# Performance work log

Hardware: AMD Instinct MI355X
Metric: run time of the kernel (lower is better)

## Reference

```python
import jax, jax.numpy as jnp
import numpy as np

HEADS = 8
DHEAD = 64
A_SCALE = 8.0  # cosine-attention logit scale (a=8 in source)
ROPE_BASE = 10000.0


def _mp_weight(w, centered):
    # Magnitude-preserving (EDM2-style) weight: optional zero-mean over fan-in,
    # unit-norm per output row, scaled by 1/sqrt(fan_in).
    if centered:
        w = w - w.mean(axis=1, keepdims=True)
    w = w / (jnp.linalg.norm(w, axis=1, keepdims=True) + 1e-8)
    return w / jnp.sqrt(jnp.asarray(w.shape[1], w.dtype))


def _rope_cos_sin(Hs, Ws, d, dtype=jnp.float32):
    # 2D axial RoPE: first d/4 rotation pairs encode row position, last d/4 column position.
    quarter = d // 4
    freqs = 1.0 / (ROPE_BASE ** (jnp.arange(quarter, dtype=dtype) / quarter))  # [d/4]
    ah = jnp.arange(Hs, dtype=dtype)[:, None] * freqs                          # [H, d/4]
    aw = jnp.arange(Ws, dtype=dtype)[:, None] * freqs                          # [W, d/4]
    ang = jnp.concatenate([
        jnp.broadcast_to(ah[:, None, :], (Hs, Ws, quarter)),
        jnp.broadcast_to(aw[None, :, :], (Hs, Ws, quarter)),
    ], axis=-1).reshape(Hs * Ws, d // 2)                                       # [L, d/2]
    return jnp.cos(ang), jnp.sin(ang)


def _apply_rope(t, cos, sin):
    # t: [N, h, L, d]; rotate interleaved pairs.
    x1, x2 = t[..., 0::2], t[..., 1::2]
    r1 = x1 * cos - x2 * sin
    r2 = x1 * sin + x2 * cos
    return jnp.stack([r1, r2], axis=-1).reshape(t.shape)


def setup_inputs() -> dict:
    key = jax.random.key(0)
    ks = jax.random.split(key, 8)
    N, C, Hs, Ws = 8, 256, 32, 32
    E, Hc = 512, 512
    return {
        "x": jax.random.normal(ks[0], (N, C, Hs, Ws), jnp.float32),
        "w": jax.random.normal(ks[1], (N, E), jnp.float32),
        "InputGain": jax.random.uniform(ks[2], (3 * Hc,), jnp.float32),
        "ResidualGain": jax.random.uniform(ks[3], (C,), jnp.float32),
        "qkv_w": jax.random.normal(ks[4], (3 * Hc, C), jnp.float32),
        "qkv_b": jnp.zeros((3 * Hc,), jnp.float32),
        "mod_w": jax.random.normal(ks[5], (E, C), jnp.float32) / jnp.sqrt(512.0),
        "proj_w": jax.random.normal(ks[6], (C, Hc), jnp.float32),
        "sinks": jnp.zeros((HEADS,), jnp.float32),
    }


def reference(x, w, InputGain, ResidualGain, qkv_w, qkv_b, mod_w, proj_w, sinks):
    N, C, Hs, Ws = x.shape
    L = Hs * Ws
    Hc = qkv_w.shape[0] // 3

    # --- fused QKV: style-modulated, biased, centered 1x1 conv with per-out-channel gain ---
    style = w @ mod_w + 1.0                                   # [N, C]
    Wq = _mp_weight(qkv_w, centered=True)                     # [3Hc, C]
    xm = x * style[:, :, None, None]
    y = jnp.einsum('nchw,oc->nohw', xm, Wq)
    y = (y + qkv_b[None, :, None, None]) * InputGain[None, :, None, None]  # [N, 3Hc, H, W]

    # --- split heads, flatten space: [N, h, L, d] ---
    y = y.reshape(N, 3, HEADS, DHEAD, L)
    q = jnp.transpose(y[:, 0], (0, 1, 3, 2))
    k = jnp.transpose(y[:, 1], (0, 1, 3, 2))
    v = jnp.transpose(y[:, 2], (0, 1, 3, 2))

    # --- 2D RoPE on q, k ---
    cos, sin = _rope_cos_sin(Hs, Ws, DHEAD, x.dtype)
    q = _apply_rope(q, cos, sin)
    k = _apply_rope(k, cos, sin)

    # --- cosine attention with per-head sink logit ---
    qn = q / (jnp.linalg.norm(q, axis=-1, keepdims=True) + 1e-8)
    kn = k / (jnp.linalg.norm(k, axis=-1, keepdims=True) + 1e-8)
    logits = A_SCALE * jnp.einsum('nhld,nhmd->nhlm', qn, kn)  # [N, h, L, L]
    sink = jnp.broadcast_to(sinks[None, :, None, None], (N, HEADS, L, 1))
    probs = jax.nn.softmax(jnp.concatenate([logits, sink], axis=-1), axis=-1)[..., :L]
    o = jnp.einsum('nhlm,nhmd->nhld', probs, v)               # [N, h, L, d]

    # --- merge heads back to map, centered 1x1 projection with per-out-channel gain ---
    o = jnp.transpose(o, (0, 1, 3, 2)).reshape(N, Hc, Hs, Ws)
    Wp = _mp_weight(proj_w, centered=True) * ResidualGain[:, None]  # [C, Hc]
    out = jnp.einsum('nchw,oc->nohw', o, Wp)
    return x + out
```

## Files before the change

### kernel.cpp

```cpp
#include <hip/hip_runtime.h>
#include <hip/hip_bf16.h>
#include <math.h>

#define NN 8
#define CC 256
#define LL 1024
#define EE 512
#define HEADS 8
#define DH 64

#define OFF_STYLE   0u
#define OFF_BIAS    2048u
#define OFF_COS     3584u
#define OFF_SIN     36352u
#define OFF_WQB     69120u
#define OFF_WPB     265728u
#define OFF_XMT     331264u
#define OFF_Q       1379840u
#define OFF_K       3476992u
#define OFF_V       5574144u
#define OFF_O       7671296u

typedef __bf16 bf16x8 __attribute__((ext_vector_type(8)));
typedef __bf16 bf16x4 __attribute__((ext_vector_type(4)));
typedef short s16x4 __attribute__((ext_vector_type(4)));
typedef float f32x4 __attribute__((ext_vector_type(4)));

__global__ __launch_bounds__(256) void k_style(const float* __restrict__ w,
                                               const float* __restrict__ mod_w,
                                               float* __restrict__ style) {
    int n  = blockIdx.x >> 2;
    int cg = blockIdx.x & 3;
    int wv = threadIdx.x >> 6, lane = threadIdx.x & 63;
    int c = cg * 64 + lane;
    __shared__ float red[4][64];
    float acc = 0.f;
    #pragma unroll 8
    for (int e = wv * 128; e < wv * 128 + 128; ++e)
        acc += w[n * EE + e] * mod_w[e * CC + c];
    red[wv][lane] = acc;
    __syncthreads();
    if (wv == 0)
        style[n * CC + c] = red[0][lane] + red[1][lane] + red[2][lane] + red[3][lane] + 1.0f;
}

__global__ __launch_bounds__(256) void k_prep_wq(const float* __restrict__ qkv_w,
                                                 const float* __restrict__ gain,
                                                 const float* __restrict__ bias,
                                                 __hip_bfloat16* __restrict__ wqb,
                                                 float* __restrict__ biasg) {
    int wv = threadIdx.x >> 6, lane = threadIdx.x & 63;
    int o = blockIdx.x * 4 + wv;
    float4 v = *reinterpret_cast<const float4*>(qkv_w + o * CC + lane * 4);
    float s = v.x + v.y + v.z + v.w;
    #pragma unroll
    for (int off = 1; off < 64; off <<= 1) s += __shfl_xor(s, off);
    float mean = s * (1.0f / 256.0f);
    float c0 = v.x - mean, c1 = v.y - mean, c2 = v.z - mean, c3 = v.w - mean;
    float ss = c0 * c0 + c1 * c1 + c2 * c2 + c3 * c3;
    #pragma unroll
    for (int off = 1; off < 64; off <<= 1) ss += __shfl_xor(ss, off);
    float g = gain[o];
    float scale = g / ((sqrtf(ss) + 1e-8f) * 16.0f);
    bf16x4 outv;
    outv[0] = (__bf16)(c0 * scale); outv[1] = (__bf16)(c1 * scale);
    outv[2] = (__bf16)(c2 * scale); outv[3] = (__bf16)(c3 * scale);
    *reinterpret_cast<bf16x4*>((__bf16*)wqb + o * CC + lane * 4) = outv;
    if (lane == 0) biasg[o] = bias[o] * g;
}

__global__ __launch_bounds__(256) void k_prep_wp(const float* __restrict__ proj_w,
                                                 const float* __restrict__ rgain,
                                                 __hip_bfloat16* __restrict__ wpb) {
    int wv = threadIdx.x >> 6, lane = threadIdx.x & 63;
    int r = blockIdx.x * 4 + wv;
    const float* p = proj_w + r * 512 + lane * 8;
    float4 v0 = *reinterpret_cast<const float4*>(p);
    float4 v1 = *reinterpret_cast<const float4*>(p + 4);
    float s = v0.x + v0.y + v0.z + v0.w + v1.x + v1.y + v1.z + v1.w;
    #pragma unroll
    for (int off = 1; off < 64; off <<= 1) s += __shfl_xor(s, off);
    float mean = s * (1.0f / 512.0f);
    float c[8] = {v0.x - mean, v0.y - mean, v0.z - mean, v0.w - mean,
                  v1.x - mean, v1.y - mean, v1.z - mean, v1.w - mean};
    float ss = 0.f;
    #pragma unroll
    for (int i = 0; i < 8; ++i) ss += c[i] * c[i];
    #pragma unroll
    for (int off = 1; off < 64; off <<= 1) ss += __shfl_xor(ss, off);
    float scale = rgain[r] / ((sqrtf(ss) + 1e-8f) * 22.62741699796952f);
    bf16x8 outv;
    #pragma unroll
    for (int i = 0; i < 8; ++i) outv[i] = (__bf16)(c[i] * scale);
    *reinterpret_cast<bf16x8*>((__bf16*)wpb + r * 512 + lane * 8) = outv;
}

__global__ __launch_bounds__(256) void k_rope(float* __restrict__ cosT, float* __restrict__ sinT) {
    int idx = blockIdx.x * 256 + threadIdx.x;
    int l = idx >> 4, j = idx & 15;
    int hh = l >> 5, ww = l & 31;
    float f = exp2f(-(float)j * 0.8304820238941836f);
    float s1, c1, s2, c2;
    __sincosf((float)hh * f, &s1, &c1);
    __sincosf((float)ww * f, &s2, &c2);
    cosT[l * 32 + j]      = c1;
    sinT[l * 32 + j]      = s1;
    cosT[l * 32 + 16 + j] = c2;
    sinT[l * 32 + 16 + j] = s2;
}

__global__ __launch_bounds__(256) void k_xm(const float* __restrict__ x,
                                            const float* __restrict__ style,
                                            __hip_bfloat16* __restrict__ xmT) {
    int lb = blockIdx.x;
    int cb = blockIdx.y;
    int n  = blockIdx.z;
    int t = threadIdx.x;
    __shared__ float tile[64][68];
    int r = t >> 2, q = t & 3;
    float st = style[n * CC + cb * 64 + r];
    const float* xp = x + (size_t)n * (CC * LL) + (size_t)(cb * 64 + r) * LL + lb * 64 + q * 16;
    #pragma unroll
    for (int i = 0; i < 4; ++i) {
        float4 v = *reinterpret_cast<const float4*>(xp + i * 4);
        tile[r][q * 16 + i * 4 + 0] = v.x * st;
        tile[r][q * 16 + i * 4 + 1] = v.y * st;
        tile[r][q * 16 + i * 4 + 2] = v.z * st;
        tile[r][q * 16 + i * 4 + 3] = v.w * st;
    }
    __syncthreads();
    __hip_bfloat16 outv[16];
    #pragma unroll
    for (int i = 0; i < 16; ++i)
        outv[i] = __float2bfloat16(tile[q * 16 + i][r]);
    __hip_bfloat16* dst = xmT + (size_t)n * (LL * CC) + (size_t)(lb * 64 + r) * CC + cb * 64 + q * 16;
    *reinterpret_cast<bf16x8*>(dst)     = *reinterpret_cast<bf16x8*>(&outv[0]);
    *reinterpret_cast<bf16x8*>(dst + 8) = *reinterpret_cast<bf16x8*>(&outv[8]);
}

__global__ __launch_bounds__(256) void k_qkv3(const __hip_bfloat16* __restrict__ wqb,
                                              const __hip_bfloat16* __restrict__ xmT,
                                              const float* __restrict__ biasg,
                                              const float* __restrict__ cosT,
                                              const float* __restrict__ sinT,
                                              __hip_bfloat16* __restrict__ qb,
                                              __hip_bfloat16* __restrict__ kb,
                                              __hip_bfloat16* __restrict__ vt) {
    int lb = blockIdx.x;
    int ob = blockIdx.y;
    int n  = blockIdx.z;
    int tid = threadIdx.x;
    int wid = tid >> 6, lane = tid & 63;
    int wr = wid >> 1, wc = wid & 1;
    int g = lane >> 4, r16 = lane & 15;

    int o0 = ob * 128 + wr * 64;
    int l0 = lb * 128 + wc * 64;
    int part = o0 >> 9;
    int h = (o0 & 511) >> 6;

    __shared__ __hip_bfloat16 smem[32768];

    const int srow[4] = {tid >> 3, (tid + 256) >> 3, (tid + 512) >> 3, (tid + 768) >> 3};
    const int scol = (tid & 7) * 8;
    int sswz[4];
    #pragma unroll
    for (int i = 0; i < 4; ++i) sswz[i] = scol ^ ((srow[i] & 7) << 3);

    const __hip_bfloat16* Agl = wqb + (size_t)(ob * 128) * CC;
    const __hip_bfloat16* Bgl = xmT + (size_t)n * (LL * CC) + (size_t)(lb * 128) * CC;

    bf16x8 ar[4], br[4];
    #pragma unroll
    for (int i = 0; i < 4; ++i) {
        ar[i] = *reinterpret_cast<const bf16x8*>(Agl + (size_t)srow[i] * CC + scol);
        br[i] = *reinterpret_cast<const bf16x8*>(Bgl + (size_t)srow[i] * CC + scol);
    }
    #pragma unroll
    for (int i = 0; i < 4; ++i) {
        *reinterpret_cast<bf16x8*>(&smem[srow[i] * 64 + sswz[i]]) = ar[i];
        *reinterpret_cast<bf16x8*>(&smem[16384 + srow[i] * 64 + sswz[i]]) = br[i];
    }
    __syncthreads();

    f32x4 acc[4][4] = {};
    int cur = 0;
    for (int t = 0; t < 4; ++t) {
        if (t < 3) {
            int kt1 = (t + 1) * 64;
            #pragma unroll
            for (int i = 0; i < 4; ++i) {
                ar[i] = *reinterpret_cast<const bf16x8*>(Agl + (size_t)srow[i] * CC + kt1 + scol);
                br[i] = *reinterpret_cast<const bf16x8*>(Bgl + (size_t)srow[i] * CC + kt1 + scol);
            }
        }
        const __hip_bfloat16* At = &smem[cur * 8192];
        const __hip_bfloat16* Bt = &smem[16384 + cur * 8192];
        #pragma unroll
        for (int kk = 0; kk < 2; ++kk) {
            int col = (kk * 32 + g * 8) ^ ((r16 & 7) << 3);
            bf16x8 a[4], b[4];
            #pragma unroll
            for (int m = 0; m < 4; ++m)
                a[m] = *reinterpret_cast<const bf16x8*>(&At[(wr * 64 + m * 16 + r16) * 64 + col]);
            #pragma unroll
            for (int nn = 0; nn < 4; ++nn)
                b[nn] = *reinterpret_cast<const bf16x8*>(&Bt[(wc * 64 + nn * 16 + r16) * 64 + col]);
            __builtin_amdgcn_s_setprio(1);
            #pragma unroll
            for (int m = 0; m < 4; ++m)
                #pragma unroll
                for (int nn = 0; nn < 4; ++nn)
                    acc[m][nn] = __builtin_amdgcn_mfma_f32_16x16x32_bf16(a[m], b[nn], acc[m][nn], 0, 0, 0);
            __builtin_amdgcn_s_setprio(0);
        }
        __syncthreads();
        if (t < 3) {
            #pragma unroll
            for (int i = 0; i < 4; ++i) {
                *reinterpret_cast<bf16x8*>(&smem[(cur ^ 1) * 8192 + srow[i] * 64 + sswz[i]]) = ar[i];
                *reinterpret_cast<bf16x8*>(&smem[16384 + (cur ^ 1) * 8192 + srow[i] * 64 + sswz[i]]) = br[i];
            }
            __syncthreads();
        }
        cur ^= 1;
    }
    __syncthreads();

    __hip_bfloat16 (*sw)[64][72] = reinterpret_cast<__hip_bfloat16 (*)[64][72]>(smem);

    float bg[4][4];
    #pragma unroll
    for (int m = 0; m < 4; ++m)
        #pragma unroll
        for (int reg = 0; reg < 4; ++reg)
            bg[m][reg] = biasg[o0 + m * 16 + 4 * g + reg];

    size_t head = (size_t)(n * 8 + h);

    if (part < 2) {
        __hip_bfloat16* dst = (part == 0) ? qb : kb;
        #pragma unroll
        for (int nn = 0; nn < 4; ++nn) {
            int l = l0 + nn * 16 + r16;
            float rv[4][4];
            float ss = 0.f;
            #pragma unroll
            for (int m = 0; m < 4; ++m) {
                int j0 = m * 8 + g * 2;
                float cA = cosT[l * 32 + j0],     sA = sinT[l * 32 + j0];
                float cB = cosT[l * 32 + j0 + 1], sB = sinT[l * 32 + j0 + 1];
                float x0 = acc[m][nn][0] + bg[m][0];
                float x1 = acc[m][nn][1] + bg[m][1];
                float x2 = acc[m][nn][2] + bg[m][2];
                float x3 = acc[m][nn][3] + bg[m][3];
                rv[m][0] = x0 * cA - x1 * sA;
                rv[m][1] = x0 * sA + x1 * cA;
                rv[m][2] = x2 * cB - x3 * sB;
                rv[m][3] = x2 * sB + x3 * cB;
                ss += rv[m][0] * rv[m][0] + rv[m][1] * rv[m][1] +
                      rv[m][2] * rv[m][2] + rv[m][3] * rv[m][3];
            }
            ss += __shfl_xor(ss, 16);
            ss += __shfl_xor(ss, 32);
            float inv = 1.0f / (sqrtf(ss) + 1e-8f);
            #pragma unroll
            for (int m = 0; m < 4; ++m)
                #pragma unroll
                for (int reg = 0; reg < 4; ++reg)
                    sw[wid][nn * 16 + r16][m * 16 + 4 * g + reg] =
                        __float2bfloat16(rv[m][reg] * inv);
        }
        #pragma unroll
        for (int it = 0; it < 8; ++it) {
            int idx = lane + it * 64;
            int ll = idx >> 3, ch = idx & 7;
            bf16x8 v = *reinterpret_cast<bf16x8*>(&sw[wid][ll][ch * 8]);
            *reinterpret_cast<bf16x8*>(dst + (head * LL + l0 + ll) * DH + ch * 8) = v;
        }
    } else {
        #pragma unroll
        for (int nn = 0; nn < 4; ++nn)
            #pragma unroll
            for (int m = 0; m < 4; ++m)
                #pragma unroll
                for (int reg = 0; reg < 4; ++reg)
                    sw[wid][m * 16 + 4 * g + reg][nn * 16 + r16] =
                        __float2bfloat16(acc[m][nn][reg] + bg[m][reg]);
        #pragma unroll
        for (int it = 0; it < 8; ++it) {
            int idx = lane + it * 64;
            int dd = idx >> 3, ch = idx & 7;
            bf16x8 v = *reinterpret_cast<bf16x8*>(&sw[wid][dd][ch * 8]);
            *reinterpret_cast<bf16x8*>(vt + (head * DH + dd) * LL + l0 + ch * 8) = v;
        }
    }
}

__global__ __launch_bounds__(256) void k_attn_mfma(
    const __hip_bfloat16* __restrict__ qb, const __hip_bfloat16* __restrict__ kb,
    const __hip_bfloat16* __restrict__ vt, const float* __restrict__ sinks,
    __hip_bfloat16* __restrict__ ob) {
    int bid = blockIdx.x;
    int swz = (bid & 7) * 64 + (bid >> 3);
    int n    = swz >> 6;
    int h    = (swz >> 3) & 7;
    int qblk = swz & 7;
    int tid  = threadIdx.x;
    int wid  = tid >> 6, lane = tid & 63;
    int g = lane >> 4, r16 = lane & 15;

    size_t head = (size_t)(n * 8 + h);
    const __hip_bfloat16* Q = qb + head * (size_t)(LL * DH);
    const __hip_bfloat16* K = kb + head * (size_t)(LL * DH);
    const __hip_bfloat16* V = vt + head * (size_t)(DH * LL);
    __hip_bfloat16* O = ob + (size_t)n * (LL * 512) + h * 64;

    int q0 = qblk * 128 + wid * 32;

    __shared__ __hip_bfloat16 kls[2][64][64];
    __shared__ __hip_bfloat16 vls[2][64][64];

    const int cl0 = tid >> 3,        cd0 = (tid & 7) * 8;
    const int cl1 = (tid + 256) >> 3, cd1 = (tid & 7) * 8;
    const int ksw0 = cd0 ^ ((cl0 & 7) << 3);
    const int ksw1 = cd1 ^ ((cl1 & 7) << 3);

    bf16x8 qf[2][2];
    #pragma unroll
    for (int qm = 0; qm < 2; ++qm)
        #pragma unroll
        for (int dc = 0; dc < 2; ++dc)
            qf[qm][dc] = *reinterpret_cast<const bf16x8*>(
                Q + (size_t)(q0 + qm * 16 + r16) * DH + dc * 32 + g * 8);

    float snk = sinks[h];
    float m = fmaxf(8.0f, snk);
    const float c1 = 8.0f * 1.44269504f;
    const float c0 = -m * 1.44269504f;

    f32x4 oacc[2][4];
    #pragma unroll
    for (int qm = 0; qm < 2; ++qm)
        #pragma unroll
        for (int dn = 0; dn < 4; ++dn)
            oacc[qm][dn] = (f32x4){0.f, 0.f, 0.f, 0.f};
    float ssum[2] = {0.f, 0.f};

    bf16x8 kr0, kr1, vr0, vr1;
    kr0 = *reinterpret_cast<const bf16x8*>(K + (size_t)cl0 * DH + cd0);
    kr1 = *reinterpret_cast<const bf16x8*>(K + (size_t)cl1 * DH + cd1);
    vr0 = *reinterpret_cast<const bf16x8*>(V + (size_t)cl0 * LL + cd0);
    vr1 = *reinterpret_cast<const bf16x8*>(V + (size_t)cl1 * LL + cd1);
    *reinterpret_cast<bf16x8*>(&kls[0][cl0][ksw0]) = kr0;
    *reinterpret_cast<bf16x8*>(&kls[0][cl1][ksw1]) = kr1;
    *reinterpret_cast<bf16x8*>(&vls[0][cl0][ksw0]) = vr0;
    *reinterpret_cast<bf16x8*>(&vls[0][cl1][ksw1]) = vr1;
    __syncthreads();

    int cur = 0;
    for (int t = 0; t < 16; ++t) {
        if (t < 15) {
            int kt1 = t * 64 + 64;
            kr0 = *reinterpret_cast<const bf16x8*>(K + (size_t)(kt1 + cl0) * DH + cd0);
            kr1 = *reinterpret_cast<const bf16x8*>(K + (size_t)(kt1 + cl1) * DH + cd1);
            vr0 = *reinterpret_cast<const bf16x8*>(V + (size_t)cl0 * LL + kt1 + cd0);
            vr1 = *reinterpret_cast<const bf16x8*>(V + (size_t)cl1 * LL + kt1 + cd1);
        }
        f32x4 sacc[2][4];
        #pragma unroll
        for (int qm = 0; qm < 2; ++qm)
            #pragma unroll
            for (int kn = 0; kn < 4; ++kn)
                sacc[qm][kn] = (f32x4){0.f, 0.f, 0.f, 0.f};
        __builtin_amdgcn_s_setprio(1);
        #pragma unroll
        for (int kn = 0; kn < 4; ++kn) {
            #pragma unroll
            for (int dc = 0; dc < 2; ++dc) {
                bf16x8 kf = *reinterpret_cast<const bf16x8*>(
                    &kls[cur][kn * 16 + r16][(dc * 32 + g * 8) ^ ((r16 & 7) << 3)]);
                #pragma unroll
                for (int qm = 0; qm < 2; ++qm)
                    sacc[qm][kn] = __builtin_amdgcn_mfma_f32_16x16x32_bf16(
                        kf, qf[qm][dc], sacc[qm][kn], 0, 0, 0);
            }
        }
        __builtin_amdgcn_s_setprio(0);
        #pragma unroll
        for (int kn = 0; kn < 4; ++kn) {
            s16x4 pa[2];
            #pragma unroll
            for (int qm = 0; qm < 2; ++qm) {
                float p0 = exp2f(fmaf(sacc[qm][kn][0], c1, c0));
                float p1 = exp2f(fmaf(sacc[qm][kn][1], c1, c0));
                float p2 = exp2f(fmaf(sacc[qm][kn][2], c1, c0));
                float p3 = exp2f(fmaf(sacc[qm][kn][3], c1, c0));
                ssum[qm] += p0 + p1 + p2 + p3;
                bf16x4 pb;
                pb[0] = (__bf16)p0; pb[1] = (__bf16)p1;
                pb[2] = (__bf16)p2; pb[3] = (__bf16)p3;
                pa[qm] = __builtin_bit_cast(s16x4, pb);
            }
            __builtin_amdgcn_s_setprio(1);
            #pragma unroll
            for (int dn = 0; dn < 4; ++dn) {
                s16x4 vb = *reinterpret_cast<const s16x4*>(
                    &vls[cur][dn * 16 + r16][(kn * 16 + g * 4) ^ ((r16 & 7) << 3)]);
                #pragma unroll
                for (int qm = 0; qm < 2; ++qm)
                    oacc[qm][dn] = __builtin_amdgcn_mfma_f32_16x16x16bf16_1k(
                        pa[qm], vb, oacc[qm][dn], 0, 0, 0);
            }
            __builtin_amdgcn_s_setprio(0);
        }
        __syncthreads();
        if (t < 15) {
            *reinterpret_cast<bf16x8*>(&kls[cur ^ 1][cl0][ksw0]) = kr0;
            *reinterpret_cast<bf16x8*>(&kls[cur ^ 1][cl1][ksw1]) = kr1;
            *reinterpret_cast<bf16x8*>(&vls[cur ^ 1][cl0][ksw0]) = vr0;
            *reinterpret_cast<bf16x8*>(&vls[cur ^ 1][cl1][ksw1]) = vr1;
            __syncthreads();
        }
        cur ^= 1;
    }

    float sink_e = exp2f((snk - m) * 1.44269504f);
    float inv[2];
    #pragma unroll
    for (int qm = 0; qm < 2; ++qm) {
        float s = ssum[qm];
        s += __shfl_xor(s, 16);
        s += __shfl_xor(s, 32);
        inv[qm] = 1.0f / (s + sink_e);
    }
    #pragma unroll
    for (int qm = 0; qm < 2; ++qm) {
        #pragma unroll
        for (int reg = 0; reg < 4; ++reg) {
            float invq = __shfl(inv[qm], 4 * g + reg);
            #pragma unroll
            for (int dn = 0; dn < 4; ++dn)
                O[(size_t)(q0 + qm * 16 + 4 * g + reg) * 512 + dn * 16 + r16] =
                    __float2bfloat16(oacc[qm][dn][reg] * invq);
        }
    }
}

__global__ __launch_bounds__(256) void k_proj3(const __hip_bfloat16* __restrict__ wpb,
                                               const __hip_bfloat16* __restrict__ ob,
                                               const float* __restrict__ x,
                                               float* __restrict__ out) {
    int lb = blockIdx.x;
    int cb = blockIdx.y;
    int n  = blockIdx.z;
    int tid = threadIdx.x;
    int wid = tid >> 6, lane = tid & 63;
    int wr = wid >> 1, wc = wid & 1;
    int g = lane >> 4, r16 = lane & 15;

    int c0 = cb * 64 + wr * 32;
    int l0 = lb * 128 + wc * 64;

    __shared__ __hip_bfloat16 smem[24576];

    const int arow[2] = {tid >> 3, (tid + 256) >> 3};
    const int brow[4] = {tid >> 3, (tid + 256) >> 3, (tid + 512) >> 3, (tid + 768) >> 3};
    const int scol = (tid & 7) * 8;
    int aswz[2], bswz[4];
    #pragma unroll
    for (int i = 0; i < 2; ++i) aswz[i] = scol ^ ((arow[i] & 7) << 3);
    #pragma unroll
    for (int i = 0; i < 4; ++i) bswz[i] = scol ^ ((brow[i] & 7) << 3);

    const __hip_bfloat16* Agl = wpb + (size_t)(cb * 64) * 512;
    const __hip_bfloat16* Bgl = ob + (size_t)n * (LL * 512) + (size_t)(lb * 128) * 512;

    bf16x8 ar[2], br[4];
    #pragma unroll
    for (int i = 0; i < 2; ++i)
        ar[i] = *reinterpret_cast<const bf16x8*>(Agl + (size_t)arow[i] * 512 + scol);
    #pragma unroll
    for (int i = 0; i < 4; ++i)
        br[i] = *reinterpret_cast<const bf16x8*>(Bgl + (size_t)brow[i] * 512 + scol);
    #pragma unroll
    for (int i = 0; i < 2; ++i)
        *reinterpret_cast<bf16x8*>(&smem[arow[i] * 64 + aswz[i]]) = ar[i];
    #pragma unroll
    for (int i = 0; i < 4; ++i)
        *reinterpret_cast<bf16x8*>(&smem[8192 + brow[i] * 64 + bswz[i]]) = br[i];
    __syncthreads();

    f32x4 acc[2][4] = {};
    int cur = 0;
    for (int t = 0; t < 8; ++t) {
        if (t < 7) {
            int kt1 = (t + 1) * 64;
            #pragma unroll
            for (int i = 0; i < 2; ++i)
                ar[i] = *reinterpret_cast<const bf16x8*>(Agl + (size_t)arow[i] * 512 + kt1 + scol);
            #pragma unroll
            for (int i = 0; i < 4; ++i)
                br[i] = *reinterpret_cast<const bf16x8*>(Bgl + (size_t)brow[i] * 512 + kt1 + scol);
        }
        const __hip_bfloat16* At = &smem[cur * 4096];
        const __hip_bfloat16* Bt = &smem[8192 + cur * 8192];
        #pragma unroll
        for (int kk = 0; kk < 2; ++kk) {
            int col = (kk * 32 + g * 8) ^ ((r16 & 7) << 3);
            bf16x8 a[2], b[4];
            #pragma unroll
            for (int m = 0; m < 2; ++m)
                a[m] = *reinterpret_cast<const bf16x8*>(&At[(wr * 32 + m * 16 + r16) * 64 + col]);
            #pragma unroll
            for (int nn = 0; nn < 4; ++nn)
                b[nn] = *reinterpret_cast<const bf16x8*>(&Bt[(wc * 64 + nn * 16 + r16) * 64 + col]);
            __builtin_amdgcn_s_setprio(1);
            #pragma unroll
            for (int m = 0; m < 2; ++m)
                #pragma unroll
                for (int nn = 0; nn < 4; ++nn)
                    acc[m][nn] = __builtin_amdgcn_mfma_f32_16x16x32_bf16(a[m], b[nn], acc[m][nn], 0, 0, 0);
            __builtin_amdgcn_s_setprio(0);
        }
        __syncthreads();
        if (t < 7) {
            #pragma unroll
            for (int i = 0; i < 2; ++i)
                *reinterpret_cast<bf16x8*>(&smem[(cur ^ 1) * 4096 + arow[i] * 64 + aswz[i]]) = ar[i];
            #pragma unroll
            for (int i = 0; i < 4; ++i)
                *reinterpret_cast<bf16x8*>(&smem[8192 + (cur ^ 1) * 8192 + brow[i] * 64 + bswz[i]]) = br[i];
            __syncthreads();
        }
        cur ^= 1;
    }

    #pragma unroll
    for (int m = 0; m < 2; ++m) {
        #pragma unroll
        for (int reg = 0; reg < 4; ++reg) {
            int c = c0 + m * 16 + 4 * g + reg;
            #pragma unroll
            for (int nn = 0; nn < 4; ++nn) {
                int l = l0 + nn * 16 + r16;
                size_t idx = (size_t)n * (CC * LL) + (size_t)c * LL + l;
                out[idx] = x[idx] + acc[m][nn][reg];
            }
        }
    }
}

extern "C" void kernel_launch(void* const* d_in, const int* in_sizes, int n_in,
                              void* d_out, int out_size, void* d_ws, size_t ws_size,
                              hipStream_t stream) {
    const float* x       = (const float*)d_in[0];
    const float* w       = (const float*)d_in[1];
    const float* igain   = (const float*)d_in[2];
    const float* rgain   = (const float*)d_in[3];
    const float* qkv_w   = (const float*)d_in[4];
    const float* qkv_b   = (const float*)d_in[5];
    const float* mod_w   = (const float*)d_in[6];
    const float* proj_w  = (const float*)d_in[7];
    const float* sinks   = (const float*)d_in[8];
    float* out = (float*)d_out;
    float* ws  = (float*)d_ws;

    float* style = ws + OFF_STYLE;
    float* biasg = ws + OFF_BIAS;
    float* cosT  = ws + OFF_COS;
    float* sinT  = ws + OFF_SIN;
    __hip_bfloat16* wqb = (__hip_bfloat16*)(ws + OFF_WQB);
    __hip_bfloat16* wpb = (__hip_bfloat16*)(ws + OFF_WPB);
    __hip_bfloat16* xmT = (__hip_bfloat16*)(ws + OFF_XMT);
    __hip_bfloat16* qb  = (__hip_bfloat16*)(ws + OFF_Q);
    __hip_bfloat16* kb  = (__hip_bfloat16*)(ws + OFF_K);
    __hip_bfloat16* vt  = (__hip_bfloat16*)(ws + OFF_V);
    __hip_bfloat16* obuf = (__hip_bfloat16*)(ws + OFF_O);

    k_style<<<32, 256, 0, stream>>>(w, mod_w, style);
    k_prep_wq<<<384, 256, 0, stream>>>(qkv_w, igain, qkv_b, wqb, biasg);
    k_prep_wp<<<64, 256, 0, stream>>>(proj_w, rgain, wpb);
    k_rope<<<64, 256, 0, stream>>>(cosT, sinT);
    k_xm<<<dim3(16, 4, NN), 256, 0, stream>>>(x, style, xmT);
    k_qkv3<<<dim3(8, 12, NN), 256, 0, stream>>>(wqb, xmT, biasg, cosT, sinT, qb, kb, vt);
    k_attn_mfma<<<512, 256, 0, stream>>>(qb, kb, vt, sinks, obuf);
    k_proj3<<<dim3(8, 4, NN), 256, 0, stream>>>(wpb, obuf, x, out);
}
```

Measured before the change: 91.79 us.

## Split attention KV range across two wave groups and merge prep kernels

The attention kernel now runs 512 threads per block. Two groups of four waves each process half of the key/value sequence with their own double-buffered LDS tiles, then merge partial outputs and row sums through shared memory before normalizing. This doubles the waves available to hide latency and halves the serial key loop per wave, at the cost of more LDS, a combine step and possibly lower occupancy. The four small weight, RoPE and style prep kernels are also fused into one launch to cut launch overhead.

```diff
diff --git a/kernel.cpp b/kernel.cpp
--- a/kernel.cpp
+++ b/kernel.cpp
@@ -26,87 +26,81 @@
 typedef short s16x4 __attribute__((ext_vector_type(4)));
 typedef float f32x4 __attribute__((ext_vector_type(4)));
 
-__global__ __launch_bounds__(256) void k_style(const float* __restrict__ w,
-                                               const float* __restrict__ mod_w,
-                                               float* __restrict__ style) {
-    int n  = blockIdx.x >> 2;
-    int cg = blockIdx.x & 3;
-    int wv = threadIdx.x >> 6, lane = threadIdx.x & 63;
-    int c = cg * 64 + lane;
-    __shared__ float red[4][64];
-    float acc = 0.f;
-    #pragma unroll 8
-    for (int e = wv * 128; e < wv * 128 + 128; ++e)
-        acc += w[n * EE + e] * mod_w[e * CC + c];
-    red[wv][lane] = acc;
-    __syncthreads();
-    if (wv == 0)
-        style[n * CC + c] = red[0][lane] + red[1][lane] + red[2][lane] + red[3][lane] + 1.0f;
-}
-
-__global__ __launch_bounds__(256) void k_prep_wq(const float* __restrict__ qkv_w,
-                                                 const float* __restrict__ gain,
-                                                 const float* __restrict__ bias,
-                                                 __hip_bfloat16* __restrict__ wqb,
-                                                 float* __restrict__ biasg) {
-    int wv = threadIdx.x >> 6, lane = threadIdx.x & 63;
-    int o = blockIdx.x * 4 + wv;
-    float4 v = *reinterpret_cast<const float4*>(qkv_w + o * CC + lane * 4);
-    float s = v.x + v.y + v.z + v.w;
-    #pragma unroll
-    for (int off = 1; off < 64; off <<= 1) s += __shfl_xor(s, off);
-    float mean = s * (1.0f / 256.0f);
-    float c0 = v.x - mean, c1 = v.y - mean, c2 = v.z - mean, c3 = v.w - mean;
-    float ss = c0 * c0 + c1 * c1 + c2 * c2 + c3 * c3;
-    #pragma unroll
-    for (int off = 1; off < 64; off <<= 1) ss += __shfl_xor(ss, off);
-    float g = gain[o];
-    float scale = g / ((sqrtf(ss) + 1e-8f) * 16.0f);
-    bf16x4 outv;
-    outv[0] = (__bf16)(c0 * scale); outv[1] = (__bf16)(c1 * scale);
-    outv[2] = (__bf16)(c2 * scale); outv[3] = (__bf16)(c3 * scale);
-    *reinterpret_cast<bf16x4*>((__bf16*)wqb + o * CC + lane * 4) = outv;
-    if (lane == 0) biasg[o] = bias[o] * g;
-}
-
-__global__ __launch_bounds__(256) void k_prep_wp(const float* __restrict__ proj_w,
-                                                 const float* __restrict__ rgain,
-                                                 __hip_bfloat16* __restrict__ wpb) {
-    int wv = threadIdx.x >> 6, lane = threadIdx.x & 63;
-    int r = blockIdx.x * 4 + wv;
-    const float* p = proj_w + r * 512 + lane * 8;
-    float4 v0 = *reinterpret_cast<const float4*>(p);
-    float4 v1 = *reinterpret_cast<const float4*>(p + 4);
-    float s = v0.x + v0.y + v0.z + v0.w + v1.x + v1.y + v1.z + v1.w;
-    #pragma unroll
-    for (int off = 1; off < 64; off <<= 1) s += __shfl_xor(s, off);
-    float mean = s * (1.0f / 512.0f);
-    float c[8] = {v0.x - mean, v0.y - mean, v0.z - mean, v0.w - mean,
-                  v1.x - mean, v1.y - mean, v1.z - mean, v1.w - mean};
-    float ss = 0.f;
-    #pragma unroll
-    for (int i = 0; i < 8; ++i) ss += c[i] * c[i];
-    #pragma unroll
-    for (int off = 1; off < 64; off <<= 1) ss += __shfl_xor(ss, off);
-    float scale = rgain[r] / ((sqrtf(ss) + 1e-8f) * 22.62741699796952f);
-    bf16x8 outv;
-    #pragma unroll
-    for (int i = 0; i < 8; ++i) outv[i] = (__bf16)(c[i] * scale);
-    *reinterpret_cast<bf16x8*>((__bf16*)wpb + r * 512 + lane * 8) = outv;
-}
-
-__global__ __launch_bounds__(256) void k_rope(float* __restrict__ cosT, float* __restrict__ sinT) {
-    int idx = blockIdx.x * 256 + threadIdx.x;
-    int l = idx >> 4, j = idx & 15;
-    int hh = l >> 5, ww = l & 31;
-    float f = exp2f(-(float)j * 0.8304820238941836f);
-    float s1, c1, s2, c2;
-    __sincosf((float)hh * f, &s1, &c1);
-    __sincosf((float)ww * f, &s2, &c2);
-    cosT[l * 32 + j]      = c1;
-    sinT[l * 32 + j]      = s1;
-    cosT[l * 32 + 16 + j] = c2;
-    sinT[l * 32 + 16 + j] = s2;
+__global__ __launch_bounds__(256) void k_prep(
+    const float* __restrict__ w, const float* __restrict__ mod_w, float* __restrict__ style,
+    const float* __restrict__ qkv_w, const float* __restrict__ gain,
+    const float* __restrict__ bias, __hip_bfloat16* __restrict__ wqb, float* __restrict__ biasg,
+    const float* __restrict__ proj_w, const float* __restrict__ rgain,
+    __hip_bfloat16* __restrict__ wpb,
+    float* __restrict__ cosT, float* __restrict__ sinT) {
+    int bid = blockIdx.x;
+    int t = threadIdx.x;
+    int wv = t >> 6, lane = t & 63;
+    if (bid < 384) {
+        int o = bid * 4 + wv;
+        float4 v = *reinterpret_cast<const float4*>(qkv_w + o * CC + lane * 4);
+        float s = v.x + v.y + v.z + v.w;
+        #pragma unroll
+        for (int off = 1; off < 64; off <<= 1) s += __shfl_xor(s, off);
+        float mean = s * (1.0f / 256.0f);
+        float c0 = v.x - mean, c1 = v.y - mean, c2 = v.z - mean, c3 = v.w - mean;
+        float ss = c0 * c0 + c1 * c1 + c2 * c2 + c3 * c3;
+        #pragma unroll
+        for (int off = 1; off < 64; off <<= 1) ss += __shfl_xor(ss, off);
+        float g = gain[o];
+        float scale = g / ((sqrtf(ss) + 1e-8f) * 16.0f);
+        bf16x4 outv;
+        outv[0] = (__bf16)(c0 * scale); outv[1] = (__bf16)(c1 * scale);
+        outv[2] = (__bf16)(c2 * scale); outv[3] = (__bf16)(c3 * scale);
+        *reinterpret_cast<bf16x4*>((__bf16*)wqb + o * CC + lane * 4) = outv;
+        if (lane == 0) biasg[o] = bias[o] * g;
+    } else if (bid < 448) {
+        int r = (bid - 384) * 4 + wv;
+        const float* p = proj_w + r * 512 + lane * 8;
+        float4 v0 = *reinterpret_cast<const float4*>(p);
+        float4 v1 = *reinterpret_cast<const float4*>(p + 4);
+        float s = v0.x + v0.y + v0.z + v0.w + v1.x + v1.y + v1.z + v1.w;
+        #pragma unroll
+        for (int off = 1; off < 64; off <<= 1) s += __shfl_xor(s, off);
+        float mean = s * (1.0f / 512.0f);
+        float c[8] = {v0.x - mean, v0.y - mean, v0.z - mean, v0.w - mean,
+                      v1.x - mean, v1.y - mean, v1.z - mean, v1.w - mean};
+        float ss = 0.f;
+        #pragma unroll
+        for (int i = 0; i < 8; ++i) ss += c[i] * c[i];
+        #pragma unroll
+        for (int off = 1; off < 64; off <<= 1) ss += __shfl_xor(ss, off);
+        float scale = rgain[r] / ((sqrtf(ss) + 1e-8f) * 22.62741699796952f);
+        bf16x8 outv;
+        #pragma unroll
+        for (int i = 0; i < 8; ++i) outv[i] = (__bf16)(c[i] * scale);
+        *reinterpret_cast<bf16x8*>((__bf16*)wpb + r * 512 + lane * 8) = outv;
+    } else if (bid < 512) {
+        int idx = (bid - 448) * 256 + t;
+        int l = idx >> 4, j = idx & 15;
+        int hh = l >> 5, ww = l & 31;
+        float f = exp2f(-(float)j * 0.8304820238941836f);
+        float s1, c1, s2, c2;
+        __sincosf((float)hh * f, &s1, &c1);
+        __sincosf((float)ww * f, &s2, &c2);
+        cosT[l * 32 + j]      = c1;
+        sinT[l * 32 + j]      = s1;
+        cosT[l * 32 + 16 + j] = c2;
+        sinT[l * 32 + 16 + j] = s2;
+    } else {
+        int b = bid - 512;
+        int n = b >> 2, cg = b & 3;
+        int c = cg * 64 + lane;
+        __shared__ float red[4][64];
+        float acc = 0.f;
+        #pragma unroll 8
+        for (int e = wv * 128; e < wv * 128 + 128; ++e)
+            acc += w[n * EE + e] * mod_w[e * CC + c];
+        red[wv][lane] = acc;
+        __syncthreads();
+        if (wv == 0)
+            style[n * CC + c] = red[0][lane] + red[1][lane] + red[2][lane] + red[3][lane] + 1.0f;
+    }
 }
 
 __global__ __launch_bounds__(256) void k_xm(const float* __restrict__ x,
@@ -297,7 +291,7 @@
     }
 }
 
-__global__ __launch_bounds__(256) void k_attn_mfma(
+__global__ __launch_bounds__(512) void k_attn_mfma(
     const __hip_bfloat16* __restrict__ qb, const __hip_bfloat16* __restrict__ kb,
     const __hip_bfloat16* __restrict__ vt, const float* __restrict__ sinks,
     __hip_bfloat16* __restrict__ ob) {
@@ -308,6 +302,8 @@
     int qblk = swz & 7;
     int tid  = threadIdx.x;
     int wid  = tid >> 6, lane = tid & 63;
+    int hf   = wid >> 2;
+    int w4   = wid & 3;
     int g = lane >> 4, r16 = lane & 15;
 
     size_t head = (size_t)(n * 8 + h);
@@ -316,15 +312,18 @@
     const __hip_bfloat16* V = vt + head * (size_t)(DH * LL);
     __hip_bfloat16* O = ob + (size_t)n * (LL * 512) + h * 64;
 
-    int q0 = qblk * 128 + wid * 32;
-
-    __shared__ __hip_bfloat16 kls[2][64][64];
-    __shared__ __hip_bfloat16 vls[2][64][64];
-
-    const int cl0 = tid >> 3,        cd0 = (tid & 7) * 8;
-    const int cl1 = (tid + 256) >> 3, cd1 = (tid & 7) * 8;
-    const int ksw0 = cd0 ^ ((cl0 & 7) << 3);
-    const int ksw1 = cd1 ^ ((cl1 & 7) << 3);
+    int q0 = qblk * 128 + w4 * 32;
+    int kbase = hf * 512;
+
+    __shared__ __hip_bfloat16 smem[32768];
+    __hip_bfloat16* kbuf[2] = { &smem[(hf * 2 + 0) * 4096], &smem[(hf * 2 + 1) * 4096] };
+    __hip_bfloat16* vbuf[2] = { &smem[16384 + (hf * 2 + 0) * 4096],
+                                &smem[16384 + (hf * 2 + 1) * 4096] };
+
+    int htid = tid & 255;
+    const int cl0 = htid >> 3, cl1 = cl0 + 32;
+    const int cd  = (htid & 7) * 8;
+    const int sw8 = cd ^ ((cl0 & 7) << 3);
 
     bf16x8 qf[2][2];
     #pragma unroll
@@ -348,24 +347,24 @@
     float ssum[2] = {0.f, 0.f};
 
     bf16x8 kr0, kr1, vr0, vr1;
-    kr0 = *reinterpret_cast<const bf16x8*>(K + (size_t)cl0 * DH + cd0);
-    kr1 = *reinterpret_cast<const bf16x8*>(K + (size_t)cl1 * DH + cd1);
-    vr0 = *reinterpret_cast<const bf16x8*>(V + (size_t)cl0 * LL + cd0);
-    vr1 = *reinterpret_cast<const bf16x8*>(V + (size_t)cl1 * LL + cd1);
-    *reinterpret_cast<bf16x8*>(&kls[0][cl0][ksw0]) = kr0;
-    *reinterpret_cast<bf16x8*>(&kls[0][cl1][ksw1]) = kr1;
-    *reinterpret_cast<bf16x8*>(&vls[0][cl0][ksw0]) = vr0;
-    *reinterpret_cast<bf16x8*>(&vls[0][cl1][ksw1]) = vr1;
+    kr0 = *reinterpret_cast<const bf16x8*>(K + (size_t)(kbase + cl0) * DH + cd);
+    kr1 = *reinterpret_cast<const bf16x8*>(K + (size_t)(kbase + cl1) * DH + cd);
+    vr0 = *reinterpret_cast<const bf16x8*>(V + (size_t)cl0 * LL + kbase + cd);
+    vr1 = *reinterpret_cast<const bf16x8*>(V + (size_t)cl1 * LL + kbase + cd);
+    *reinterpret_cast<bf16x8*>(&kbuf[0][cl0 * 64 + sw8]) = kr0;
+    *reinterpret_cast<bf16x8*>(&kbuf[0][cl1 * 64 + sw8]) = kr1;
+    *reinterpret_cast<bf16x8*>(&vbuf[0][cl0 * 64 + sw8]) = vr0;
+    *reinterpret_cast<bf16x8*>(&vbuf[0][cl1 * 64 + sw8]) = vr1;
     __syncthreads();
 
     int cur = 0;
-    for (int t = 0; t < 16; ++t) {
-        if (t < 15) {
-            int kt1 = t * 64 + 64;
-            kr0 = *reinterpret_cast<const bf16x8*>(K + (size_t)(kt1 + cl0) * DH + cd0);
-            kr1 = *reinterpret_cast<const bf16x8*>(K + (size_t)(kt1 + cl1) * DH + cd1);
-            vr0 = *reinterpret_cast<const bf16x8*>(V + (size_t)cl0 * LL + kt1 + cd0);
-            vr1 = *reinterpret_cast<const bf16x8*>(V + (size_t)cl1 * LL + kt1 + cd1);
+    for (int t = 0; t < 8; ++t) {
+        if (t < 7) {
+            int kt1 = kbase + (t + 1) * 64;
+            kr0 = *reinterpret_cast<const bf16x8*>(K + (size_t)(kt1 + cl0) * DH + cd);
+            kr1 = *reinterpret_cast<const bf16x8*>(K + (size_t)(kt1 + cl1) * DH + cd);
+            vr0 = *reinterpret_cast<const bf16x8*>(V + (size_t)cl0 * LL + kt1 + cd);
+            vr1 = *reinterpret_cast<const bf16x8*>(V + (size_t)cl1 * LL + kt1 + cd);
         }
         f32x4 sacc[2][4];
         #pragma unroll
@@ -379,7 +378,7 @@
             #pragma unroll
             for (int dc = 0; dc < 2; ++dc) {
                 bf16x8 kf = *reinterpret_cast<const bf16x8*>(
-                    &kls[cur][kn * 16 + r16][(dc * 32 + g * 8) ^ ((r16 & 7) << 3)]);
+                    &kbuf[cur][(kn * 16 + r16) * 64 + ((dc * 32 + g * 8) ^ ((r16 & 7) << 3))]);
                 #pragma unroll
                 for (int qm = 0; qm < 2; ++qm)
                     sacc[qm][kn] = __builtin_amdgcn_mfma_f32_16x16x32_bf16(
@@ -406,7 +405,7 @@
             #pragma unroll
             for (int dn = 0; dn < 4; ++dn) {
                 s16x4 vb = *reinterpret_cast<const s16x4*>(
-                    &vls[cur][dn * 16 + r16][(kn * 16 + g * 4) ^ ((r16 & 7) << 3)]);
+                    &vbuf[cur][(dn * 16 + r16) * 64 + ((kn * 16 + g * 4) ^ ((r16 & 7) << 3))]);
                 #pragma unroll
                 for (int qm = 0; qm < 2; ++qm)
                     oacc[qm][dn] = __builtin_amdgcn_mfma_f32_16x16x16bf16_1k(
@@ -415,34 +414,57 @@
             __builtin_amdgcn_s_setprio(0);
         }
         __syncthreads();
-        if (t < 15) {
-            *reinterpret_cast<bf16x8*>(&kls[cur ^ 1][cl0][ksw0]) = kr0;
-            *reinterpret_cast<bf16x8*>(&kls[cur ^ 1][cl1][ksw1]) = kr1;
-            *reinterpret_cast<bf16x8*>(&vls[cur ^ 1][cl0][ksw0]) = vr0;
-            *reinterpret_cast<bf16x8*>(&vls[cur ^ 1][cl1][ksw1]) = vr1;
+        if (t < 7) {
+            *reinterpret_cast<bf16x8*>(&kbuf[cur ^ 1][cl0 * 64 + sw8]) = kr0;
+            *reinterpret_cast<bf16x8*>(&kbuf[cur ^ 1][cl1 * 64 + sw8]) = kr1;
+            *reinterpret_cast<bf16x8*>(&vbuf[cur ^ 1][cl0 * 64 + sw8]) = vr0;
+            *reinterpret_cast<bf16x8*>(&vbuf[cur ^ 1][cl1 * 64 + sw8]) = vr1;
             __syncthreads();
         }
         cur ^= 1;
     }
 
-    float sink_e = exp2f((snk - m) * 1.44269504f);
-    float inv[2];
-    #pragma unroll
-    for (int qm = 0; qm < 2; ++qm) {
-        float s = ssum[qm];
-        s += __shfl_xor(s, 16);
-        s += __shfl_xor(s, 32);
-        inv[qm] = 1.0f / (s + sink_e);
-    }
-    #pragma unroll
-    for (int qm = 0; qm < 2; ++qm) {
-        #pragma unroll
-        for (int reg = 0; reg < 4; ++reg) {
-            float invq = __shfl(inv[qm], 4 * g + reg);
+    float* cmb = reinterpret_cast<float*>(smem);
+    if (hf == 1) {
+        float* p = cmb + (size_t)(w4 * 64 + lane) * 36;
+        #pragma unroll
+        for (int qm = 0; qm < 2; ++qm)
             #pragma unroll
             for (int dn = 0; dn < 4; ++dn)
-                O[(size_t)(q0 + qm * 16 + 4 * g + reg) * 512 + dn * 16 + r16] =
-                    __float2bfloat16(oacc[qm][dn][reg] * invq);
+                *reinterpret_cast<f32x4*>(p + qm * 16 + dn * 4) = oacc[qm][dn];
+        p[32] = ssum[0];
+        p[33] = ssum[1];
+    }
+    __syncthreads();
+    if (hf == 0) {
+        float* p = cmb + (size_t)(w4 * 64 + lane) * 36;
+        #pragma unroll
+        for (int qm = 0; qm < 2; ++qm)
+            #pragma unroll
+            for (int dn = 0; dn < 4; ++dn)
+                oacc[qm][dn] += *reinterpret_cast<f32x4*>(p + qm * 16 + dn * 4);
+        ssum[0] += p[32];
+        ssum[1] += p[33];
+
+        float sink_e = exp2f((snk - m) * 1.44269504f);
+        float inv[2];
+        #pragma unroll
+        for (int qm = 0; qm < 2; ++qm) {
+            float s = ssum[qm];
+            s += __shfl_xor(s, 16);
+            s += __shfl_xor(s, 32);
+            inv[qm] = 1.0f / (s + sink_e);
+        }
+        #pragma unroll
+        for (int qm = 0; qm < 2; ++qm) {
+            #pragma unroll
+            for (int reg = 0; reg < 4; ++reg) {
+                float invq = __shfl(inv[qm], 4 * g + reg);
+                #pragma unroll
+                for (int dn = 0; dn < 4; ++dn)
+                    O[(size_t)(q0 + qm * 16 + 4 * g + reg) * 512 + dn * 16 + r16] =
+                        __float2bfloat16(oacc[qm][dn][reg] * invq);
+            }
         }
     }
 }
@@ -578,12 +600,10 @@
     __hip_bfloat16* vt  = (__hip_bfloat16*)(ws + OFF_V);
     __hip_bfloat16* obuf = (__hip_bfloat16*)(ws + OFF_O);
 
-    k_style<<<32, 256, 0, stream>>>(w, mod_w, style);
-    k_prep_wq<<<384, 256, 0, stream>>>(qkv_w, igain, qkv_b, wqb, biasg);
-    k_prep_wp<<<64, 256, 0, stream>>>(proj_w, rgain, wpb);
-    k_rope<<<64, 256, 0, stream>>>(cosT, sinT);
+    k_prep<<<544, 256, 0, stream>>>(w, mod_w, style, qkv_w, igain, qkv_b, wqb, biasg,
+                                    proj_w, rgain, wpb, cosT, sinT);
     k_xm<<<dim3(16, 4, NN), 256, 0, stream>>>(x, style, xmT);
     k_qkv3<<<dim3(8, 12, NN), 256, 0, stream>>>(wqb, xmT, biasg, cosT, sinT, qb, kb, vt);
-    k_attn_mfma<<<512, 256, 0, stream>>>(qb, kb, vt, sinks, obuf);
+    k_attn_mfma<<<512, 512, 0, stream>>>(qb, kb, vt, sinks, obuf);
     k_proj3<<<dim3(8, 4, NN), 256, 0, stream>>>(wpb, obuf, x, out);
 }
```

Result: slower. 95.61 us (+4.2%).
